# Performance work log

Hardware: AMD Instinct MI355X
Metric: run time of the kernel (lower is better)

The kernel has to match this reference:

```python
import jax, jax.numpy as jnp
import numpy as np

B, C, N, S = 4, 64, 16384, 16
DIM_OUT = 64
SCALE = DIM_OUT ** (-0.5)


def setup_inputs() -> dict:
    key = jax.random.key(0)
    ks = jax.random.split(key, 8)
    return {
        "xyz": jax.random.normal(ks[0], (B, 3, N), dtype=jnp.float32),
        "neighbor_xyz": jax.random.normal(ks[1], (B, 3, N, S), dtype=jnp.float32),
        "points": jax.random.normal(ks[2], (B, C, N), dtype=jnp.float32),
        "neighbor_points": jax.random.normal(ks[3], (B, C, N, S), dtype=jnp.float32),
        "Wk": jax.random.normal(ks[4], (C, C), dtype=jnp.float32) * 0.05,
        "Wv": jax.random.normal(ks[5], (DIM_OUT, C + 3), dtype=jnp.float32) * 0.05,
        "Wp": jax.random.normal(ks[6], (C, 4), dtype=jnp.float32) * 0.05,
        "bp": jax.random.normal(ks[7], (C,), dtype=jnp.float32) * 0.05,
    }


def reference(xyz, neighbor_xyz, points, neighbor_points, Wk, Wv, Wp, bp):
    # relative position of each neighbor: [B,3,N,S]
    tmp = xyz[:, :, :, None] - neighbor_xyz
    xyz_norm = jnp.sqrt(jnp.sum(tmp * tmp, axis=1, keepdims=True))  # [B,1,N,S]
    pos = jnp.concatenate([tmp, xyz_norm], axis=1)  # [B,4,N,S]

    # 1x1 convs == per-point channel matmuls
    pos_enc = jnp.einsum('oc,bcns->bons', Wp, pos) + bp[None, :, None, None]
    k = jnp.einsum('oc,bcns->bons', Wk, neighbor_points + pos_enc)  # [B,C,N,S]
    v_in = jnp.concatenate([neighbor_points, tmp], axis=1)  # [B,C+3,N,S]
    v = jnp.einsum('oc,bcns->bons', Wv, v_in)  # [B,dim_out,N,S]

    q = points * SCALE  # [B,C,N]
    attn = jax.nn.softmax(jnp.einsum('bcn,bcns->bns', q, k), axis=-1)  # [B,N,S]
    out = jnp.einsum('bns,bcns->bcn', attn, v)  # [B,dim_out,N]
    return out
```

## Files before the change

### kernel.cpp

```cpp
#include <hip/hip_runtime.h>
#include <math.h>

constexpr int Nn = 16384;
constexpr int ST = 68;
constexpr size_t NS = (size_t)Nn * 16;
constexpr int GPB = 8;

template <int CTRL>
__device__ __forceinline__ float dpp_f(float x) {
    return __int_as_float(
        __builtin_amdgcn_update_dpp(0, __float_as_int(x), CTRL, 0xF, 0xF, false));
}
__device__ __forceinline__ float qsum4(float v) {
    v += dpp_f<0xB1>(v);
    v += dpp_f<0x4E>(v);
    return v;
}
__device__ __forceinline__ float qmax4(float v) {
    v = fmaxf(v, dpp_f<0xB1>(v));
    v = fmaxf(v, dpp_f<0x4E>(v));
    return v;
}

#define BAR() do { asm volatile("s_waitcnt lgkmcnt(0)" ::: "memory"); \
    __builtin_amdgcn_s_barrier(); asm volatile("" ::: "memory"); } while (0)

__global__ __launch_bounds__(256, 4) void qkpp_kernel(
    const float* __restrict__ points, const float* __restrict__ Wk,
    const float* __restrict__ Wp, float* __restrict__ ws)
{
    const int tid = threadIdx.x;
    const int lane = tid & 63;
    const int q = lane >> 4;
    const int pt = blockIdx.x * 64 + (tid >> 6) * 16 + (lane & 15);
    const int b = pt >> 14;
    const int n = pt & (Nn - 1);

    float qk[16];
#pragma unroll
    for (int k = 0; k < 16; ++k) qk[k] = 0.f;

    const float* prow = points + (size_t)b * 64 * Nn + n;
    const float* wkq = Wk + 16 * q;
#pragma unroll 4
    for (int c = 0; c < 64; ++c) {
        const float qv = prow[(size_t)c * Nn];
        const float4 w0 = *(const float4*)(wkq + c * 64 + 0);
        const float4 w1 = *(const float4*)(wkq + c * 64 + 4);
        const float4 w2 = *(const float4*)(wkq + c * 64 + 8);
        const float4 w3 = *(const float4*)(wkq + c * 64 + 12);
        qk[0]  = fmaf(qv, w0.x, qk[0]);  qk[1]  = fmaf(qv, w0.y, qk[1]);
        qk[2]  = fmaf(qv, w0.z, qk[2]);  qk[3]  = fmaf(qv, w0.w, qk[3]);
        qk[4]  = fmaf(qv, w1.x, qk[4]);  qk[5]  = fmaf(qv, w1.y, qk[5]);
        qk[6]  = fmaf(qv, w1.z, qk[6]);  qk[7]  = fmaf(qv, w1.w, qk[7]);
        qk[8]  = fmaf(qv, w2.x, qk[8]);  qk[9]  = fmaf(qv, w2.y, qk[9]);
        qk[10] = fmaf(qv, w2.z, qk[10]); qk[11] = fmaf(qv, w2.w, qk[11]);
        qk[12] = fmaf(qv, w3.x, qk[12]); qk[13] = fmaf(qv, w3.y, qk[13]);
        qk[14] = fmaf(qv, w3.z, qk[14]); qk[15] = fmaf(qv, w3.w, qk[15]);
    }
#pragma unroll
    for (int k = 0; k < 16; ++k) qk[k] *= 0.125f;

    float p0 = 0.f, p1 = 0.f, p2 = 0.f, p3 = 0.f;
#pragma unroll
    for (int k = 0; k < 16; ++k) {
        const float4 wp4 = *(const float4*)(Wp + (16 * q + k) * 4);
        p0 = fmaf(qk[k], wp4.x, p0);
        p1 = fmaf(qk[k], wp4.y, p1);
        p2 = fmaf(qk[k], wp4.z, p2);
        p3 = fmaf(qk[k], wp4.w, p3);
    }
    p0 += __shfl_xor(p0, 16); p0 += __shfl_xor(p0, 32);
    p1 += __shfl_xor(p1, 16); p1 += __shfl_xor(p1, 32);
    p2 += __shfl_xor(p2, 16); p2 += __shfl_xor(p2, 32);
    p3 += __shfl_xor(p3, 16); p3 += __shfl_xor(p3, 32);

    float* orow = ws + (size_t)pt * ST + 16 * q;
    ((float4*)orow)[0] = make_float4(qk[0],  qk[1],  qk[2],  qk[3]);
    ((float4*)orow)[1] = make_float4(qk[4],  qk[5],  qk[6],  qk[7]);
    ((float4*)orow)[2] = make_float4(qk[8],  qk[9],  qk[10], qk[11]);
    ((float4*)orow)[3] = make_float4(qk[12], qk[13], qk[14], qk[15]);
    if (q == 0)
        *(float4*)(ws + (size_t)pt * ST + 64) = make_float4(p0, p1, p2, p3);
}

__global__ __launch_bounds__(256, 2) void attn_out_kernel(
    const float* __restrict__ xyz, const float* __restrict__ nxyz,
    const float* __restrict__ npts, const float* __restrict__ Wv,
    const float* __restrict__ ws, float* __restrict__ out)
{
    __shared__ float wvT[67 * 68];
    __shared__ __align__(16) float lexch[4][64][4];
    __shared__ float vbexch[67 * 17];

    const int tid = threadIdx.x;
    const int w = tid >> 6;
    const int l = tid & 63;
    const int p = l >> 2;
    const int sq = l & 3;

    const int gptbase = blockIdx.x * (16 * GPB);
    const int b = gptbase >> 14;
    const int ngbase = gptbase & (Nn - 1);

    for (int idx = tid; idx < 64 * 67; idx += 256) {
        const int o = idx / 67, c = idx - o * 67;
        wvT[c * 68 + o] = Wv[idx];
    }

    const float* npb0 = npts + ((size_t)(b * 64 + 16 * w)) * NS + (size_t)ngbase * 16 + 4 * l;

    float4 npA[16], npB[16], qqA[4], qqB[4], nxA[3], nxB[3];
    float4 ppA = make_float4(0,0,0,0), ppB = make_float4(0,0,0,0);
    float xA[3] = {0,0,0}, xB[3] = {0,0,0};

    auto prefetch = [&](int g, float4 (&np)[16], float4 (&qq)[4],
                        float4 (&nx)[3], float (&xx)[3], float4& pp) {
        const float* npb = npb0 + (size_t)g * 256;
#pragma unroll
        for (int k = 0; k < 16; ++k) np[k] = *(const float4*)(npb + (size_t)k * NS);
        const float* qrow = ws + (size_t)(gptbase + 16 * g + p) * ST + 16 * w;
        qq[0] = ((const float4*)qrow)[0];
        qq[1] = ((const float4*)qrow)[1];
        qq[2] = ((const float4*)qrow)[2];
        qq[3] = ((const float4*)qrow)[3];
        if (w == 3) {
            const int ng = ngbase + 16 * g;
            nx[0] = *(const float4*)(nxyz + ((size_t)(b * 3 + 0) * Nn + ng) * 16 + 4 * l);
            nx[1] = *(const float4*)(nxyz + ((size_t)(b * 3 + 1) * Nn + ng) * 16 + 4 * l);
            nx[2] = *(const float4*)(nxyz + ((size_t)(b * 3 + 2) * Nn + ng) * 16 + 4 * l);
            xx[0] = xyz[(size_t)(b * 3 + 0) * Nn + ng + p];
            xx[1] = xyz[(size_t)(b * 3 + 1) * Nn + ng + p];
            xx[2] = xyz[(size_t)(b * 3 + 2) * Nn + ng + p];
            pp = *(const float4*)(ws + (size_t)(gptbase + 16 * g + p) * ST + 64);
        }
    };

    auto step = [&](int g, float4 (&np)[16], float4 (&qq)[4],
                    float4 (&nx)[3], float (&xx)[3], float4& pp) {
        const int ng = ngbase + 16 * g;

        float4 d04 = make_float4(0,0,0,0), d14 = d04, d24 = d04, dn4 = d04;
        if (w == 3) {
            d04 = make_float4(xx[0] - nx[0].x, xx[0] - nx[0].y, xx[0] - nx[0].z, xx[0] - nx[0].w);
            d14 = make_float4(xx[1] - nx[1].x, xx[1] - nx[1].y, xx[1] - nx[1].z, xx[1] - nx[1].w);
            d24 = make_float4(xx[2] - nx[2].x, xx[2] - nx[2].y, xx[2] - nx[2].z, xx[2] - nx[2].w);
            dn4 = make_float4(sqrtf(d04.x * d04.x + d14.x * d14.x + d24.x * d24.x),
                              sqrtf(d04.y * d04.y + d14.y * d14.y + d24.y * d24.y),
                              sqrtf(d04.z * d04.z + d14.z * d14.z + d24.z * d24.z),
                              sqrtf(d04.w * d04.w + d14.w * d14.w + d24.w * d24.w));
        }

        const float qks[16] = {qq[0].x, qq[0].y, qq[0].z, qq[0].w,
                               qq[1].x, qq[1].y, qq[1].z, qq[1].w,
                               qq[2].x, qq[2].y, qq[2].z, qq[2].w,
                               qq[3].x, qq[3].y, qq[3].z, qq[3].w};
        float4 lp = make_float4(0.f, 0.f, 0.f, 0.f);
#pragma unroll
        for (int k = 0; k < 16; ++k) {
            lp.x = fmaf(qks[k], np[k].x, lp.x);
            lp.y = fmaf(qks[k], np[k].y, lp.y);
            lp.z = fmaf(qks[k], np[k].z, lp.z);
            lp.w = fmaf(qks[k], np[k].w, lp.w);
        }
        if (w == 3) {
            lp.x += pp.x * d04.x + pp.y * d14.x + pp.z * d24.x + pp.w * dn4.x;
            lp.y += pp.x * d04.y + pp.y * d14.y + pp.z * d24.y + pp.w * dn4.y;
            lp.z += pp.x * d04.z + pp.y * d14.z + pp.z * d24.z + pp.w * dn4.z;
            lp.w += pp.x * d04.w + pp.y * d14.w + pp.z * d24.w + pp.w * dn4.w;
        }

        BAR();
        *(float4*)&lexch[w][l][0] = lp;
        BAR();
        const float4 g0 = *(const float4*)&lexch[0][l][0];
        const float4 g1 = *(const float4*)&lexch[1][l][0];
        const float4 g2 = *(const float4*)&lexch[2][l][0];
        const float4 g3 = *(const float4*)&lexch[3][l][0];
        const float4 lg = make_float4(g0.x + g1.x + g2.x + g3.x,
                                      g0.y + g1.y + g2.y + g3.y,
                                      g0.z + g1.z + g2.z + g3.z,
                                      g0.w + g1.w + g2.w + g3.w);

        float mx = fmaxf(fmaxf(lg.x, lg.y), fmaxf(lg.z, lg.w));
        mx = qmax4(mx);
        const float e0 = __expf(lg.x - mx), e1 = __expf(lg.y - mx);
        const float e2 = __expf(lg.z - mx), e3 = __expf(lg.w - mx);
        const float se = qsum4((e0 + e1) + (e2 + e3));
        const float inv = 1.0f / se;
        const float at0 = e0 * inv, at1 = e1 * inv, at2 = e2 * inv, at3 = e3 * inv;

#pragma unroll
        for (int k = 0; k < 16; ++k) {
            float v = at0 * np[k].x + at1 * np[k].y + at2 * np[k].z + at3 * np[k].w;
            v = qsum4(v);
            if (sq == (k & 3)) vbexch[(16 * w + k) * 17 + p] = v;
        }
        if (w == 3) {
            const float t0 = qsum4(at0 * d04.x + at1 * d04.y + at2 * d04.z + at3 * d04.w);
            const float t1 = qsum4(at0 * d14.x + at1 * d14.y + at2 * d14.z + at3 * d14.w);
            const float t2 = qsum4(at0 * d24.x + at1 * d24.y + at2 * d24.z + at3 * d24.w);
            if (sq == 0) vbexch[64 * 17 + p] = t0;
            else if (sq == 1) vbexch[65 * 17 + p] = t1;
            else if (sq == 2) vbexch[66 * 17 + p] = t2;
        }
        BAR();

        float4 oa = make_float4(0.f, 0.f, 0.f, 0.f);
#pragma unroll
        for (int c = 0; c < 67; ++c) {
            const float vb = vbexch[c * 17 + p];
            const float4 wq = *(const float4*)&wvT[c * 68 + 16 * w + 4 * sq];
            oa.x = fmaf(vb, wq.x, oa.x);
            oa.y = fmaf(vb, wq.y, oa.y);
            oa.z = fmaf(vb, wq.z, oa.z);
            oa.w = fmaf(vb, wq.w, oa.w);
        }

        float* ob = out + ((size_t)(b * 64 + 16 * w + 4 * sq)) * Nn + ng + p;
        ob[0]              = oa.x;
        ob[(size_t)Nn]     = oa.y;
        ob[(size_t)Nn * 2] = oa.z;
        ob[(size_t)Nn * 3] = oa.w;
    };

    prefetch(0, npA, qqA, nxA, xA, ppA);
#pragma unroll 1
    for (int gg = 0; gg < GPB / 2; ++gg) {
        prefetch(2 * gg + 1, npB, qqB, nxB, xB, ppB);
        step(2 * gg, npA, qqA, nxA, xA, ppA);
        if (2 * gg + 2 < GPB)
            prefetch(2 * gg + 2, npA, qqA, nxA, xA, ppA);
        step(2 * gg + 1, npB, qqB, nxB, xB, ppB);
    }
}

extern "C" void kernel_launch(void* const* d_in, const int* in_sizes, int n_in,
                              void* d_out, int out_size, void* d_ws, size_t ws_size,
                              hipStream_t stream) {
    const float* xyz    = (const float*)d_in[0];
    const float* nxyz   = (const float*)d_in[1];
    const float* points = (const float*)d_in[2];
    const float* npts   = (const float*)d_in[3];
    const float* Wk     = (const float*)d_in[4];
    const float* Wv     = (const float*)d_in[5];
    const float* Wp     = (const float*)d_in[6];
    float* out = (float*)d_out;
    float* ws = (float*)d_ws;

    hipLaunchKernelGGL(qkpp_kernel,     dim3(1024), dim3(256), 0, stream,
                       points, Wk, Wp, ws);
    hipLaunchKernelGGL(attn_out_kernel, dim3(512),  dim3(256), 0, stream,
                       xyz, nxyz, npts, Wv, ws, out);
}
```

Before: 129.5 us.

## Replace double-buffered register prefetch with single buffer and raise occupancy

Drops the A/B double-buffered register prefetch in favor of a single buffer refilled after the softmax and value reduction for each group, issued before the output GEMV barrier. Points per block are halved, the grid is doubled and launch bounds are raised to three blocks per SIMD. The aim is to hide memory latency through more resident waves instead of a deep per-thread prefetch. The risk is a shorter prefetch distance and more blocks each reloading Wv into shared memory.

```diff
diff --git a/kernel.cpp b/kernel.cpp
--- a/kernel.cpp
+++ b/kernel.cpp
@@ -4,7 +4,7 @@
 constexpr int Nn = 16384;
 constexpr int ST = 68;
 constexpr size_t NS = (size_t)Nn * 16;
-constexpr int GPB = 8;
+constexpr int GPB = 4;
 
 template <int CTRL>
 __device__ __forceinline__ float dpp_f(float x) {
@@ -84,7 +84,7 @@
         *(float4*)(ws + (size_t)pt * ST + 64) = make_float4(p0, p1, p2, p3);
 }
 
-__global__ __launch_bounds__(256, 2) void attn_out_kernel(
+__global__ __launch_bounds__(256, 3) void attn_out_kernel(
     const float* __restrict__ xyz, const float* __restrict__ nxyz,
     const float* __restrict__ npts, const float* __restrict__ Wv,
     const float* __restrict__ ws, float* __restrict__ out)
@@ -98,7 +98,6 @@
     const int l = tid & 63;
     const int p = l >> 2;
     const int sq = l & 3;
-
     const int gptbase = blockIdx.x * (16 * GPB);
     const int b = gptbase >> 14;
     const int ngbase = gptbase & (Nn - 1);
@@ -110,37 +109,34 @@
 
     const float* npb0 = npts + ((size_t)(b * 64 + 16 * w)) * NS + (size_t)ngbase * 16 + 4 * l;
 
-    float4 npA[16], npB[16], qqA[4], qqB[4], nxA[3], nxB[3];
-    float4 ppA = make_float4(0,0,0,0), ppB = make_float4(0,0,0,0);
-    float xA[3] = {0,0,0}, xB[3] = {0,0,0};
-
-    auto prefetch = [&](int g, float4 (&np)[16], float4 (&qq)[4],
-                        float4 (&nx)[3], float (&xx)[3], float4& pp) {
-        const float* npb = npb0 + (size_t)g * 256;
-#pragma unroll
-        for (int k = 0; k < 16; ++k) np[k] = *(const float4*)(npb + (size_t)k * NS);
-        const float* qrow = ws + (size_t)(gptbase + 16 * g + p) * ST + 16 * w;
+    float4 npv4[16], qq[4], nx[3], pp = make_float4(0, 0, 0, 0);
+    float xx[3] = {0, 0, 0};
+    nx[0] = nx[1] = nx[2] = make_float4(0, 0, 0, 0);
+
+    {
+#pragma unroll
+        for (int k = 0; k < 16; ++k) npv4[k] = *(const float4*)(npb0 + (size_t)k * NS);
+        const float* qrow = ws + (size_t)(gptbase + p) * ST + 16 * w;
         qq[0] = ((const float4*)qrow)[0];
         qq[1] = ((const float4*)qrow)[1];
         qq[2] = ((const float4*)qrow)[2];
         qq[3] = ((const float4*)qrow)[3];
         if (w == 3) {
-            const int ng = ngbase + 16 * g;
-            nx[0] = *(const float4*)(nxyz + ((size_t)(b * 3 + 0) * Nn + ng) * 16 + 4 * l);
-            nx[1] = *(const float4*)(nxyz + ((size_t)(b * 3 + 1) * Nn + ng) * 16 + 4 * l);
-            nx[2] = *(const float4*)(nxyz + ((size_t)(b * 3 + 2) * Nn + ng) * 16 + 4 * l);
-            xx[0] = xyz[(size_t)(b * 3 + 0) * Nn + ng + p];
-            xx[1] = xyz[(size_t)(b * 3 + 1) * Nn + ng + p];
-            xx[2] = xyz[(size_t)(b * 3 + 2) * Nn + ng + p];
-            pp = *(const float4*)(ws + (size_t)(gptbase + 16 * g + p) * ST + 64);
-        }
-    };
-
-    auto step = [&](int g, float4 (&np)[16], float4 (&qq)[4],
-                    float4 (&nx)[3], float (&xx)[3], float4& pp) {
+            nx[0] = *(const float4*)(nxyz + ((size_t)(b * 3 + 0) * Nn + ngbase) * 16 + 4 * l);
+            nx[1] = *(const float4*)(nxyz + ((size_t)(b * 3 + 1) * Nn + ngbase) * 16 + 4 * l);
+            nx[2] = *(const float4*)(nxyz + ((size_t)(b * 3 + 2) * Nn + ngbase) * 16 + 4 * l);
+            xx[0] = xyz[(size_t)(b * 3 + 0) * Nn + ngbase + p];
+            xx[1] = xyz[(size_t)(b * 3 + 1) * Nn + ngbase + p];
+            xx[2] = xyz[(size_t)(b * 3 + 2) * Nn + ngbase + p];
+            pp = *(const float4*)(ws + (size_t)(gptbase + p) * ST + 64);
+        }
+    }
+
+#pragma unroll
+    for (int g = 0; g < GPB; ++g) {
         const int ng = ngbase + 16 * g;
 
-        float4 d04 = make_float4(0,0,0,0), d14 = d04, d24 = d04, dn4 = d04;
+        float4 d04 = make_float4(0, 0, 0, 0), d14 = d04, d24 = d04, dn4 = d04;
         if (w == 3) {
             d04 = make_float4(xx[0] - nx[0].x, xx[0] - nx[0].y, xx[0] - nx[0].z, xx[0] - nx[0].w);
             d14 = make_float4(xx[1] - nx[1].x, xx[1] - nx[1].y, xx[1] - nx[1].z, xx[1] - nx[1].w);
@@ -158,10 +154,10 @@
         float4 lp = make_float4(0.f, 0.f, 0.f, 0.f);
 #pragma unroll
         for (int k = 0; k < 16; ++k) {
-            lp.x = fmaf(qks[k], np[k].x, lp.x);
-            lp.y = fmaf(qks[k], np[k].y, lp.y);
-            lp.z = fmaf(qks[k], np[k].z, lp.z);
-            lp.w = fmaf(qks[k], np[k].w, lp.w);
+            lp.x = fmaf(qks[k], npv4[k].x, lp.x);
+            lp.y = fmaf(qks[k], npv4[k].y, lp.y);
+            lp.z = fmaf(qks[k], npv4[k].z, lp.z);
+            lp.w = fmaf(qks[k], npv4[k].w, lp.w);
         }
         if (w == 3) {
             lp.x += pp.x * d04.x + pp.y * d14.x + pp.z * d24.x + pp.w * dn4.x;
@@ -192,7 +188,7 @@
 
 #pragma unroll
         for (int k = 0; k < 16; ++k) {
-            float v = at0 * np[k].x + at1 * np[k].y + at2 * np[k].z + at3 * np[k].w;
+            float v = at0 * npv4[k].x + at1 * npv4[k].y + at2 * npv4[k].z + at3 * npv4[k].w;
             v = qsum4(v);
             if (sq == (k & 3)) vbexch[(16 * w + k) * 17 + p] = v;
         }
@@ -204,6 +200,28 @@
             else if (sq == 1) vbexch[65 * 17 + p] = t1;
             else if (sq == 2) vbexch[66 * 17 + p] = t2;
         }
+
+        if (g + 1 < GPB) {
+            const float* npb = npb0 + (size_t)(g + 1) * 256;
+#pragma unroll
+            for (int k = 0; k < 16; ++k) npv4[k] = *(const float4*)(npb + (size_t)k * NS);
+            const float* qrow = ws + (size_t)(gptbase + 16 * (g + 1) + p) * ST + 16 * w;
+            qq[0] = ((const float4*)qrow)[0];
+            qq[1] = ((const float4*)qrow)[1];
+            qq[2] = ((const float4*)qrow)[2];
+            qq[3] = ((const float4*)qrow)[3];
+            if (w == 3) {
+                const int ng2 = ngbase + 16 * (g + 1);
+                nx[0] = *(const float4*)(nxyz + ((size_t)(b * 3 + 0) * Nn + ng2) * 16 + 4 * l);
+                nx[1] = *(const float4*)(nxyz + ((size_t)(b * 3 + 1) * Nn + ng2) * 16 + 4 * l);
+                nx[2] = *(const float4*)(nxyz + ((size_t)(b * 3 + 2) * Nn + ng2) * 16 + 4 * l);
+                xx[0] = xyz[(size_t)(b * 3 + 0) * Nn + ng2 + p];
+                xx[1] = xyz[(size_t)(b * 3 + 1) * Nn + ng2 + p];
+                xx[2] = xyz[(size_t)(b * 3 + 2) * Nn + ng2 + p];
+                pp = *(const float4*)(ws + (size_t)(gptbase + 16 * (g + 1) + p) * ST + 64);
+            }
+        }
+
         BAR();
 
         float4 oa = make_float4(0.f, 0.f, 0.f, 0.f);
@@ -222,16 +240,6 @@
         ob[(size_t)Nn]     = oa.y;
         ob[(size_t)Nn * 2] = oa.z;
         ob[(size_t)Nn * 3] = oa.w;
-    };
-
-    prefetch(0, npA, qqA, nxA, xA, ppA);
-#pragma unroll 1
-    for (int gg = 0; gg < GPB / 2; ++gg) {
-        prefetch(2 * gg + 1, npB, qqB, nxB, xB, ppB);
-        step(2 * gg, npA, qqA, nxA, xA, ppA);
-        if (2 * gg + 2 < GPB)
-            prefetch(2 * gg + 2, npA, qqA, nxA, xA, ppA);
-        step(2 * gg + 1, npB, qqB, nxB, xB, ppB);
     }
 }
 
@@ -250,6 +258,6 @@
 
     hipLaunchKernelGGL(qkpp_kernel,     dim3(1024), dim3(256), 0, stream,
                        points, Wk, Wp, ws);
-    hipLaunchKernelGGL(attn_out_kernel, dim3(512),  dim3(256), 0, stream,
+    hipLaunchKernelGGL(attn_out_kernel, dim3(1024), dim3(256), 0, stream,
                        xyz, nxyz, npts, Wv, ws, out);
 }
```

Result: faster. 115.4 us (-10.9%).
